# Kernel optimization log

Hardware: AMD Instinct MI355X
Metric: run time of the kernel (lower is better)

Reference implementation:

```python
import jax, jax.numpy as jnp
import numpy as np

TEMPERATURE = 1.0  # init kwarg
B, D = 8192, 128


def setup_inputs() -> dict:
    key = jax.random.key(0)
    k1, k2 = jax.random.split(key)
    sk = jax.random.normal(k1, (B, D), dtype=jnp.float32)
    im = jax.random.normal(k2, (B, D), dtype=jnp.float32)
    return {"sk": sk, "im": im}


def reference(sk, im):
    # The torch module builds a [2B,2B] Euclidean distance matrix over the
    # interleaved [sk_0, im_0, sk_1, im_1, ...] rows, then via the eye-mask /
    # repeat_interleave / [:,1::2] / good_indices / [::2] gather chain selects,
    # for each anchor i, logits row = [-d(sk_i, im_i)/T] ++ [-d(sk_i, im_j)/T, j != i]
    # with label 0, followed by mean cross-entropy.  Since cross-entropy only
    # depends on {row values} and which entry is positive, this is exactly:
    #   loss = mean_i( logsumexp_j(-d(sk_i, im_j)/T) - (-d(sk_i, im_i)/T) )
    # so we only need the [B,B] sk-vs-im distance block (dist_type == 0).
    sq = (
        jnp.sum(sk * sk, axis=1)[:, None]
        + jnp.sum(im * im, axis=1)[None, :]
        - 2.0 * (sk @ im.T)
    )  # [B, B] squared distances
    d = jnp.sqrt(jnp.maximum(sq, 0.0))
    logits = -d / TEMPERATURE  # [B, B]
    lse = jax.nn.logsumexp(logits, axis=1)  # [B]
    loss = jnp.mean(lse - jnp.diagonal(logits))
    return loss
```

## Files before the change

### kernel.cpp

```cpp
#include <hip/hip_runtime.h>
#include <math.h>

#define NB 8192
#define ND 128
#define GSTEP 64
#define NSTEP 8
#define NJB 16

#define C2F 2.0813689810056077f
#define NC2 (-4.1627379620112154f)

typedef __bf16 bf16x8 __attribute__((ext_vector_type(8)));
typedef float f32x4 __attribute__((ext_vector_type(4)));

typedef __attribute__((address_space(3))) void lds_void_t;
typedef __attribute__((address_space(1))) const void gconst_void_t;

__device__ __forceinline__ unsigned f2bf(float f) {
    union { float f; unsigned u; } v; v.f = f;
    unsigned r = v.u + 0x7FFFu + ((v.u >> 16) & 1u);
    return r >> 16;
}

__global__ void __launch_bounds__(256) prep_kernel(
    const float* __restrict__ sk, const float* __restrict__ im,
    unsigned short* __restrict__ skb, unsigned short* __restrict__ imb,
    float* __restrict__ skn, float* __restrict__ imn,
    float* __restrict__ diag, float* __restrict__ gacc,
    unsigned* __restrict__ ticket) {
    if (blockIdx.x == 0 && threadIdx.x == 0) { *gacc = 0.f; *ticket = 0u; }
    const int wave = threadIdx.x >> 6, lane = threadIdx.x & 63;
    const int half = lane >> 5, l32 = lane & 31;
    const int row = blockIdx.x * 8 + wave * 2 + half;
    const size_t off = (size_t)row * ND + l32 * 4;
    const float4 a = *reinterpret_cast<const float4*>(sk + off);
    const float4 b = *reinterpret_cast<const float4*>(im + off);
    ushort4 pa, pb;
    pa.x = (unsigned short)f2bf(a.x); pa.y = (unsigned short)f2bf(a.y);
    pa.z = (unsigned short)f2bf(a.z); pa.w = (unsigned short)f2bf(a.w);
    pb.x = (unsigned short)f2bf(b.x); pb.y = (unsigned short)f2bf(b.y);
    pb.z = (unsigned short)f2bf(b.z); pb.w = (unsigned short)f2bf(b.w);
    *reinterpret_cast<ushort4*>(skb + off) = pa;
    *reinterpret_cast<ushort4*>(imb + off) = pb;
    float sa = a.x * a.x + a.y * a.y + a.z * a.z + a.w * a.w;
    float sb = b.x * b.x + b.y * b.y + b.z * b.z + b.w * b.w;
    float dx = a.x - b.x, dy = a.y - b.y, dz = a.z - b.z, dw = a.w - b.w;
    float sd = dx * dx + dy * dy + dz * dz + dw * dw;
#pragma unroll
    for (int st = 1; st < 32; st <<= 1) {
        sa += __shfl_xor(sa, st);
        sb += __shfl_xor(sb, st);
        sd += __shfl_xor(sd, st);
    }
    if (l32 == 0) {
        skn[row] = sa * C2F;
        imn[row] = sb * C2F;
        diag[row] = sqrtf(sd);
    }
}

__global__ void __launch_bounds__(256, 4) tile_kernel(
    const unsigned short* __restrict__ skb, const unsigned short* __restrict__ imb,
    const float* __restrict__ skn, const float* __restrict__ imn,
    float* __restrict__ partial) {
    __shared__ unsigned short Ast[2][GSTEP * ND];

    const int t = threadIdx.x;
    const int w = t >> 6, lane = t & 63;
    const int hi = lane >> 4, lo = lane & 15;
    const int iw = blockIdx.x * 128 + w * 32;
    const int jg0 = blockIdx.y * (GSTEP * NSTEP);

    bf16x8 bfr[2][4];
#pragma unroll
    for (int n = 0; n < 2; ++n) {
        const unsigned short* bp = skb + (size_t)(iw + n * 16 + lo) * ND + hi * 8;
#pragma unroll
        for (int kk = 0; kk < 4; ++kk)
            bfr[n][kk] = *reinterpret_cast<const bf16x8*>(bp + kk * 32);
    }
    float skv[2];
#pragma unroll
    for (int n = 0; n < 2; ++n) skv[n] = skn[iw + n * 16 + lo];

#define STAGE_A(buf, jrow0)                                                       \
    {                                                                             \
        _Pragma("unroll")                                                         \
        for (int q = 0; q < 4; ++q) {                                             \
            const int rl = w * 16 + q * 4 + hi;                                   \
            const int cs = lo ^ (rl & 15);                                        \
            const unsigned short* gp = imb + (size_t)((jrow0) + rl) * ND + cs * 8;\
            __builtin_amdgcn_global_load_lds((gconst_void_t*)gp,                  \
                (lds_void_t*)(&Ast[(buf)][(w * 16 + q * 4) * ND]), 16, 0, 0);     \
        }                                                                         \
    }

    STAGE_A(0, jg0)
    __syncthreads();

    float sacc[2] = {0.f, 0.f};

    for (int s = 0; s < NSTEP; ++s) {
        const int jb = jg0 + s * GSTEP;
        if (s + 1 < NSTEP) STAGE_A((s + 1) & 1, jb + GSTEP)

        float imnv[4][4];
#pragma unroll
        for (int m = 0; m < 4; ++m) {
            float4 v = *reinterpret_cast<const float4*>(imn + jb + m * 16 + hi * 4);
            imnv[m][0] = v.x; imnv[m][1] = v.y; imnv[m][2] = v.z; imnv[m][3] = v.w;
        }

        f32x4 acc[4][2];
#pragma unroll
        for (int m = 0; m < 4; ++m)
#pragma unroll
            for (int n = 0; n < 2; ++n)
                acc[m][n] = (f32x4){0.f, 0.f, 0.f, 0.f};

        const char* Ab = (const char*)Ast[s & 1];
#pragma unroll
        for (int kk = 0; kk < 4; ++kk) {
            const int cb = ((kk * 4 + hi) ^ lo) << 4;
            bf16x8 af[4];
#pragma unroll
            for (int m = 0; m < 4; ++m)
                af[m] = *reinterpret_cast<const bf16x8*>(Ab + (m * 16 + lo) * 256 + cb);
#pragma unroll
            for (int m = 0; m < 4; ++m)
#pragma unroll
                for (int n = 0; n < 2; ++n)
                    acc[m][n] = __builtin_amdgcn_mfma_f32_16x16x32_bf16(
                        af[m], bfr[n][kk], acc[m][n], 0, 0, 0);
        }

#pragma unroll
        for (int n = 0; n < 2; ++n) {
            float ssum = 0.f;
#pragma unroll
            for (int m = 0; m < 4; ++m) {
#pragma unroll
                for (int r = 0; r < 4; ++r) {
                    float sq2 = fmaf(NC2, acc[m][n][r], skv[n]) + imnv[m][r];
                    sq2 = fmaxf(sq2, 0.f);
                    float d2;
                    asm("v_sqrt_f32 %0, %1" : "=v"(d2) : "v"(sq2));
                    float e;
                    asm("v_exp_f32 %0, -%1" : "=v"(e) : "v"(d2));
                    ssum += e;
                }
            }
            sacc[n] += ssum;
        }
        __syncthreads();
    }

#pragma unroll
    for (int n = 0; n < 2; ++n) {
        sacc[n] += __shfl_xor(sacc[n], 16);
        sacc[n] += __shfl_xor(sacc[n], 32);
    }
    if (lane < 16) {
        partial[(size_t)blockIdx.y * NB + iw + lo] = sacc[0];
        partial[(size_t)blockIdx.y * NB + iw + 16 + lo] = sacc[1];
    }
#undef STAGE_A
}

__global__ void finalize_kernel(const float* __restrict__ partial,
                                const float* __restrict__ diag,
                                float* __restrict__ gacc, unsigned* __restrict__ ticket,
                                float* __restrict__ out) {
    const int i = blockIdx.x * 256 + threadIdx.x;
    float rs = 0.f;
#pragma unroll
    for (int c = 0; c < NJB; ++c) rs += partial[(size_t)c * NB + i];
    float v = __logf(rs) + diag[i];
    __shared__ float red[256];
    red[threadIdx.x] = v;
    __syncthreads();
    for (int st = 128; st > 0; st >>= 1) {
        if (threadIdx.x < st) red[threadIdx.x] += red[threadIdx.x + st];
        __syncthreads();
    }
    if (threadIdx.x == 0) {
        atomicAdd(gacc, red[0]);
        __threadfence();
        unsigned old = atomicAdd(ticket, 1u);
        if (old == (NB / 256) - 1) {
            float tot = atomicAdd(gacc, 0.f);
            out[0] = tot / (float)NB;
        }
    }
}

extern "C" void kernel_launch(void* const* d_in, const int* in_sizes, int n_in,
                              void* d_out, int out_size, void* d_ws, size_t ws_size,
                              hipStream_t stream) {
    const float* sk = (const float*)d_in[0];
    const float* im = (const float*)d_in[1];
    float* out = (float*)d_out;
    float* ws = (float*)d_ws;

    unsigned short* skb = (unsigned short*)ws;
    unsigned short* imb = skb + (size_t)NB * ND;
    float* fbase   = ws + (size_t)NB * ND;
    float* skn     = fbase;
    float* imn     = fbase + NB;
    float* diag    = fbase + 2 * NB;
    float* partial = fbase + 3 * NB;
    float* gacc    = partial + (size_t)NJB * NB;
    unsigned* ticket = (unsigned*)(gacc + 1);

    prep_kernel<<<NB / 8, 256, 0, stream>>>(
        sk, im, skb, imb, skn, imn, diag, gacc, ticket);
    dim3 grid(NB / 128, NJB);
    tile_kernel<<<grid, 256, 0, stream>>>(skb, imb, skn, imn, partial);
    finalize_kernel<<<NB / 256, 256, 0, stream>>>(partial, diag, gacc, ticket, out);
}
```

Measured before the change: 90.93 us.

## Switch distance GEMM from bf16 to fp8 MFMA with re-swizzled LDS layout

Quantizes sk and im to fp8 in the prep kernel and computes the Gram matrix with 16x16x32 fp8 MFMA instead of bf16, halving operand bytes in global memory and LDS and using the higher-rate fp8 matrix path. The LDS staging and swizzle are reworked for 8-byte fp8 fragments, the j-range split is doubled (NJB 32, NSTEP 4) with occupancy hint raised to 5, and the clamp is replaced by abs inside sqrt. The cost is a large loss of precision in the dot products, which may push the loss value outside tolerance.

```diff
diff --git a/kernel.cpp b/kernel.cpp
--- a/kernel.cpp
+++ b/kernel.cpp
@@ -4,13 +4,12 @@
 #define NB 8192
 #define ND 128
 #define GSTEP 64
-#define NSTEP 8
-#define NJB 16
+#define NSTEP 4
+#define NJB 32
 
 #define C2F 2.0813689810056077f
 #define NC2 (-4.1627379620112154f)
 
-typedef __bf16 bf16x8 __attribute__((ext_vector_type(8)));
 typedef float f32x4 __attribute__((ext_vector_type(4)));
 
 typedef __attribute__((address_space(3))) void lds_void_t;
@@ -24,7 +23,7 @@
 
 __global__ void __launch_bounds__(256) prep_kernel(
     const float* __restrict__ sk, const float* __restrict__ im,
-    unsigned short* __restrict__ skb, unsigned short* __restrict__ imb,
+    unsigned* __restrict__ skb8, unsigned* __restrict__ imb8,
     float* __restrict__ skn, float* __restrict__ imn,
     float* __restrict__ diag, float* __restrict__ gacc,
     unsigned* __restrict__ ticket) {
@@ -32,16 +31,16 @@
     const int wave = threadIdx.x >> 6, lane = threadIdx.x & 63;
     const int half = lane >> 5, l32 = lane & 31;
     const int row = blockIdx.x * 8 + wave * 2 + half;
-    const size_t off = (size_t)row * ND + l32 * 4;
+    const size_t off = (size_t)row * 128 + l32 * 4;
     const float4 a = *reinterpret_cast<const float4*>(sk + off);
     const float4 b = *reinterpret_cast<const float4*>(im + off);
-    ushort4 pa, pb;
-    pa.x = (unsigned short)f2bf(a.x); pa.y = (unsigned short)f2bf(a.y);
-    pa.z = (unsigned short)f2bf(a.z); pa.w = (unsigned short)f2bf(a.w);
-    pb.x = (unsigned short)f2bf(b.x); pb.y = (unsigned short)f2bf(b.y);
-    pb.z = (unsigned short)f2bf(b.z); pb.w = (unsigned short)f2bf(b.w);
-    *reinterpret_cast<ushort4*>(skb + off) = pa;
-    *reinterpret_cast<ushort4*>(imb + off) = pb;
+    unsigned pa = 0, pb = 0;
+    pa = __builtin_amdgcn_cvt_pk_fp8_f32(a.x, a.y, pa, false);
+    pa = __builtin_amdgcn_cvt_pk_fp8_f32(a.z, a.w, pa, true);
+    pb = __builtin_amdgcn_cvt_pk_fp8_f32(b.x, b.y, pb, false);
+    pb = __builtin_amdgcn_cvt_pk_fp8_f32(b.z, b.w, pb, true);
+    skb8[row * 32 + l32] = pa;
+    imb8[row * 32 + l32] = pb;
     float sa = a.x * a.x + a.y * a.y + a.z * a.z + a.w * a.w;
     float sb = b.x * b.x + b.y * b.y + b.z * b.z + b.w * b.w;
     float dx = a.x - b.x, dy = a.y - b.y, dz = a.z - b.z, dw = a.w - b.w;
@@ -59,11 +58,11 @@
     }
 }
 
-__global__ void __launch_bounds__(256, 4) tile_kernel(
-    const unsigned short* __restrict__ skb, const unsigned short* __restrict__ imb,
+__global__ void __launch_bounds__(256, 5) tile_kernel(
+    const unsigned char* __restrict__ skb8, const unsigned char* __restrict__ imb8,
     const float* __restrict__ skn, const float* __restrict__ imn,
     float* __restrict__ partial) {
-    __shared__ unsigned short Ast[2][GSTEP * ND];
+    __shared__ unsigned char Ast[2][GSTEP * ND];
 
     const int t = threadIdx.x;
     const int w = t >> 6, lane = t & 63;
@@ -71,13 +70,13 @@
     const int iw = blockIdx.x * 128 + w * 32;
     const int jg0 = blockIdx.y * (GSTEP * NSTEP);
 
-    bf16x8 bfr[2][4];
+    long bfr[2][4];
 #pragma unroll
     for (int n = 0; n < 2; ++n) {
-        const unsigned short* bp = skb + (size_t)(iw + n * 16 + lo) * ND + hi * 8;
+        const unsigned char* bp = skb8 + (size_t)(iw + n * 16 + lo) * ND + hi * 8;
 #pragma unroll
         for (int kk = 0; kk < 4; ++kk)
-            bfr[n][kk] = *reinterpret_cast<const bf16x8*>(bp + kk * 32);
+            bfr[n][kk] = *reinterpret_cast<const long*>(bp + kk * 32);
     }
     float skv[2];
 #pragma unroll
@@ -86,12 +85,12 @@
 #define STAGE_A(buf, jrow0)                                                       \
     {                                                                             \
         _Pragma("unroll")                                                         \
-        for (int q = 0; q < 4; ++q) {                                             \
-            const int rl = w * 16 + q * 4 + hi;                                   \
-            const int cs = lo ^ (rl & 15);                                        \
-            const unsigned short* gp = imb + (size_t)((jrow0) + rl) * ND + cs * 8;\
+        for (int q = 0; q < 2; ++q) {                                             \
+            const int rl = w * 16 + q * 8 + (lane >> 3);                          \
+            const int sp = (lane & 7) ^ ((rl >> 1) & 7);                          \
+            const unsigned char* gp = imb8 + (size_t)((jrow0) + rl) * ND + sp * 16;\
             __builtin_amdgcn_global_load_lds((gconst_void_t*)gp,                  \
-                (lds_void_t*)(&Ast[(buf)][(w * 16 + q * 4) * ND]), 16, 0, 0);     \
+                (lds_void_t*)(&Ast[(buf)][(w * 16 + q * 8) * ND]), 16, 0, 0);     \
         }                                                                         \
     }
 
@@ -121,16 +120,16 @@
         const char* Ab = (const char*)Ast[s & 1];
 #pragma unroll
         for (int kk = 0; kk < 4; ++kk) {
-            const int cb = ((kk * 4 + hi) ^ lo) << 4;
-            bf16x8 af[4];
+            long af[4];
 #pragma unroll
             for (int m = 0; m < 4; ++m)
-                af[m] = *reinterpret_cast<const bf16x8*>(Ab + (m * 16 + lo) * 256 + cb);
+                af[m] = *reinterpret_cast<const long*>(
+                    Ab + (m * 16 + lo) * ND + (((kk * 4 + hi) ^ (lo & 14)) << 3));
 #pragma unroll
             for (int m = 0; m < 4; ++m)
 #pragma unroll
                 for (int n = 0; n < 2; ++n)
-                    acc[m][n] = __builtin_amdgcn_mfma_f32_16x16x32_bf16(
+                    acc[m][n] = __builtin_amdgcn_mfma_f32_16x16x32_fp8_fp8(
                         af[m], bfr[n][kk], acc[m][n], 0, 0, 0);
         }
 
@@ -142,9 +141,8 @@
 #pragma unroll
                 for (int r = 0; r < 4; ++r) {
                     float sq2 = fmaf(NC2, acc[m][n][r], skv[n]) + imnv[m][r];
-                    sq2 = fmaxf(sq2, 0.f);
                     float d2;
-                    asm("v_sqrt_f32 %0, %1" : "=v"(d2) : "v"(sq2));
+                    asm("v_sqrt_f32 %0, abs(%1)" : "=v"(d2) : "v"(sq2));
                     float e;
                     asm("v_exp_f32 %0, -%1" : "=v"(e) : "v"(d2));
                     ssum += e;
@@ -202,9 +200,9 @@
     float* out = (float*)d_out;
     float* ws = (float*)d_ws;
 
-    unsigned short* skb = (unsigned short*)ws;
-    unsigned short* imb = skb + (size_t)NB * ND;
-    float* fbase   = ws + (size_t)NB * ND;
+    unsigned char* skb8 = (unsigned char*)ws;
+    unsigned char* imb8 = skb8 + (size_t)NB * ND;
+    float* fbase   = ws + (size_t)NB * ND / 2;
     float* skn     = fbase;
     float* imn     = fbase + NB;
     float* diag    = fbase + 2 * NB;
@@ -213,8 +211,8 @@
     unsigned* ticket = (unsigned*)(gacc + 1);
 
     prep_kernel<<<NB / 8, 256, 0, stream>>>(
-        sk, im, skb, imb, skn, imn, diag, gacc, ticket);
+        sk, im, (unsigned*)skb8, (unsigned*)imb8, skn, imn, diag, gacc, ticket);
     dim3 grid(NB / 128, NJB);
-    tile_kernel<<<grid, 256, 0, stream>>>(skb, imb, skn, imn, partial);
+    tile_kernel<<<grid, 256, 0, stream>>>(skb8, imb8, skn, imn, partial);
     finalize_kernel<<<NB / 256, 256, 0, stream>>>(partial, diag, gacc, ticket, out);
 }
```

Result: no change. 89.17 us (-1.9%).
